# Kernel tuning notes

Hardware: AMD Instinct MI355X
Metric: run time of the kernel (lower is better)

Reference implementation:

```python
import jax, jax.numpy as jnp
import numpy as np

HEADS = 16
D_K = 64  # hidden_size // heads = 1024 // 16
SCALE = D_K ** 0.5


def setup_inputs() -> dict:
    key = jax.random.key(0)
    ks = jax.random.split(key, 7)
    B, S, D = 4, 2048, 1024
    H = 1024  # hidden_size
    O = 1024  # outputs_dims
    s = 0.02
    return {
        "query": jax.random.normal(ks[0], (B, S, D), dtype=jnp.float32),
        "key": jax.random.normal(ks[1], (B, S, D), dtype=jnp.float32),
        "value": jax.random.normal(ks[2], (B, S, D), dtype=jnp.float32),
        "Wq": jax.random.normal(ks[3], (D, H), dtype=jnp.float32) * s,
        "Wk": jax.random.normal(ks[4], (D, H), dtype=jnp.float32) * s,
        "Wv": jax.random.normal(ks[5], (D, H), dtype=jnp.float32) * s,
        "Wo": jax.random.normal(ks[6], (H, O), dtype=jnp.float32) * s,
    }


def reference(query, key, value, Wq, Wk, Wv, Wo):
    B, S, _ = query.shape
    # Dense projections with relu activation (as in the original module)
    q = jax.nn.relu(query @ Wq).reshape(B, S, HEADS, D_K)  # [B,S,H,dk]
    k = jax.nn.relu(key @ Wk).reshape(B, S, HEADS, D_K)
    v = jax.nn.relu(value @ Wv).reshape(B, S, HEADS, D_K)
    # scores: [B,H,Sq,Sk]
    scores = jnp.einsum('bqhd,bkhd->bhqk', q, k) / SCALE
    attn = jax.nn.softmax(scores, axis=-1)
    # attention-weighted values -> [B,Sq,H,dk] -> [B,Sq,H*dk]
    ctx = jnp.einsum('bhqk,bkhd->bqhd', attn, v).reshape(B, S, HEADS * D_K)
    out = jax.nn.relu(ctx @ Wo)
    return out
```

## Files before the change

kernel.cpp:

```cpp
#include <hip/hip_runtime.h>

typedef unsigned short u16;
typedef __bf16 bf16x8 __attribute__((ext_vector_type(8)));
typedef float f32x4 __attribute__((ext_vector_type(4)));
typedef u16 u16x8 __attribute__((ext_vector_type(8)));
typedef u16 u16x4 __attribute__((ext_vector_type(4)));

#define MFMA16(a, b, c) __builtin_amdgcn_mfma_f32_16x16x32_bf16(a, b, c, 0, 0, 0)

static constexpr float QSC = 0.18033688011112042f;

__device__ inline u16 f2bf(float f) {
  union { float f; unsigned u; } x; x.f = f;
  unsigned r = x.u + 0x7FFF + ((x.u >> 16) & 1);
  return (u16)(r >> 16);
}
__device__ inline u16 cvt_bf(float f) {
  __bf16 h = (__bf16)f; return __builtin_bit_cast(u16, h);
}
__device__ inline bf16x8 ld_frag(const u16* p) {
  return __builtin_bit_cast(bf16x8, *(const u16x8*)p);
}
__device__ inline void dma16(const u16* g, u16* l) {
  __builtin_amdgcn_global_load_lds(
      (const __attribute__((address_space(1))) unsigned*)g,
      (__attribute__((address_space(3))) unsigned*)l, 16, 0, 0);
}

#if __has_builtin(__builtin_amdgcn_exp2f)
#define EXP2(x) __builtin_amdgcn_exp2f(x)
#else
#define EXP2(x) exp2f(x)
#endif

__launch_bounds__(256)
__global__ void prep_w(const float* __restrict__ Wq, const float* __restrict__ Wk,
                       const float* __restrict__ Wv, const float* __restrict__ Wo,
                       u16* __restrict__ Wt) {
  __shared__ u16 T[64 * 72];
  const int z = blockIdx.z;
  const float* W = z == 0 ? Wq : z == 1 ? Wk : z == 2 ? Wv : Wo;
  u16* D = Wt + ((size_t)z << 20);
  const int k0 = blockIdx.y * 64, c0 = blockIdx.x * 64;
  const int tid = threadIdx.x;
  const int kr = tid >> 2, cs = (tid & 3) * 16;
  const float* src = W + (size_t)(k0 + kr) * 1024 + c0 + cs;
  float f[16];
#pragma unroll
  for (int i = 0; i < 4; ++i) *(float4*)&f[i * 4] = ((const float4*)src)[i];
#pragma unroll
  for (int i = 0; i < 16; ++i) T[(cs + i) * 72 + kr] = cvt_bf(f[i]);
  __syncthreads();
  const int nn = tid >> 2, ks = (tid & 3) * 16;
  u16* dst = D + (size_t)(c0 + nn) * 1024 + k0 + ks;
  *(u16x8*)dst = *(u16x8*)&T[nn * 72 + ks];
  *(u16x8*)(dst + 8) = *(u16x8*)&T[nn * 72 + ks + 8];
}

__launch_bounds__(256)
__global__ void prep_a(const float* __restrict__ q, const float* __restrict__ k,
                       const float* __restrict__ v, u16* __restrict__ dq,
                       u16* __restrict__ dk, u16* __restrict__ dv) {
  const int z = blockIdx.z;
  const float* s = z == 0 ? q : z == 1 ? k : v;
  u16* d = z == 0 ? dq : z == 1 ? dk : dv;
  for (size_t i = blockIdx.x * 256 + threadIdx.x; i < (size_t)1048576; i += 262144) {
    const float* g = s + i * 8;
    float4 f0 = *(const float4*)g, f1 = *(const float4*)(g + 4);
    u16x8 h;
    h[0] = cvt_bf(f0.x); h[1] = cvt_bf(f0.y); h[2] = cvt_bf(f0.z); h[3] = cvt_bf(f0.w);
    h[4] = cvt_bf(f1.x); h[5] = cvt_bf(f1.y); h[6] = cvt_bf(f1.z); h[7] = cvt_bf(f1.w);
    *(u16x8*)(d + i * 8) = h;
  }
}

__launch_bounds__(256)
__global__ void gemm_fwd(const u16* __restrict__ Aq, const u16* __restrict__ Ak,
                         const u16* __restrict__ Av, const u16* __restrict__ Wt,
                         u16* __restrict__ Qw, u16* __restrict__ Kw,
                         u16* __restrict__ Vw) {
  __shared__ u16 smem[8704];
  u16* Asm = smem;
  u16* Bsm = smem + 4096;
  const int z = blockIdx.z;
  const u16* A = z == 0 ? Aq : z == 1 ? Ak : Av;
  const u16* Bt = Wt + ((size_t)z << 20);
  u16* out = z == 0 ? Qw : z == 1 ? Kw : Vw;

  const int tid = threadIdx.x;
  const int lane = tid & 63, l15 = lane & 15, quad = lane >> 4;
  const int wv = tid >> 6, wm = wv & 1, wn = wv >> 1;
  const int m0 = (blockIdx.x * 8 + (blockIdx.y >> 3)) * 128;
  const int n0 = (blockIdx.y & 7) * 128;

  f32x4 acc[4][4] = {};

  for (int k0 = 0; k0 < 1024; k0 += 32) {
    __syncthreads();
#pragma unroll
    for (int t = 0; t < 2; ++t) {
      const int cb = t * 256 + wv * 64;
      const int c = cb + lane, mn = c & 127, kc = c >> 7;
      dma16(A + (size_t)(m0 + mn) * 1024 + k0 + kc * 8, &Asm[cb * 8]);
      dma16(Bt + (size_t)(n0 + mn) * 1024 + k0 + kc * 8, &Bsm[cb * 8]);
    }
    __syncthreads();
    bf16x8 a[4], b[4];
#pragma unroll
    for (int i = 0; i < 4; ++i)
      a[i] = ld_frag(&Asm[(quad * 128 + wm * 64 + i * 16 + l15) * 8]);
#pragma unroll
    for (int j = 0; j < 4; ++j)
      b[j] = ld_frag(&Bsm[(quad * 128 + wn * 64 + j * 16 + l15) * 8]);
#pragma unroll
    for (int i = 0; i < 4; ++i)
#pragma unroll
      for (int j = 0; j < 4; ++j)
        acc[i][j] = MFMA16(a[i], b[j], acc[i][j]);
  }

  if (z < 2) {
    const float sc = z == 0 ? QSC : 1.0f;
#pragma unroll
    for (int i = 0; i < 4; ++i)
#pragma unroll
      for (int j = 0; j < 4; ++j)
#pragma unroll
        for (int r = 0; r < 4; ++r) {
          float v = fmaxf(acc[i][j][r], 0.f) * sc;
          int m = m0 + wm * 64 + i * 16 + quad * 4 + r;
          int n = n0 + wn * 64 + j * 16 + l15;
          out[(size_t)m * 1024 + n] = f2bf(v);
        }
  } else {
    const int b = m0 >> 11, s0 = m0 & 2047;
#pragma unroll
    for (int half = 0; half < 2; ++half) {
      __syncthreads();
      if (wn == half) {
#pragma unroll
        for (int i = 0; i < 4; ++i)
#pragma unroll
          for (int j = 0; j < 4; ++j) {
            u16x4 pk;
#pragma unroll
            for (int r = 0; r < 4; ++r) pk[r] = f2bf(fmaxf(acc[i][j][r], 0.f));
            const int nn = j * 16 + l15;
            const int ml = wm * 64 + i * 16 + quad * 4;
            *(u16x4*)&smem[nn * 136 + ml] = pk;
          }
      }
      __syncthreads();
      const int h = (n0 + half * 64) >> 6;
      const int nn = tid >> 2, seg = (tid & 3) * 32;
      u16* dst = out + ((size_t)((b * 16 + h) * 64 + nn)) * 2048 + s0 + seg;
#pragma unroll
      for (int i2 = 0; i2 < 4; ++i2)
        *(u16x8*)&dst[i2 * 8] = *(u16x8*)&smem[nn * 136 + seg + i2 * 8];
    }
  }
}

__launch_bounds__(256)
__global__ void gemm_out(const u16* __restrict__ A, const u16* __restrict__ Bt,
                         float* __restrict__ out) {
  __shared__ u16 smem[8192];
  u16* Asm = smem;
  u16* Bsm = smem + 4096;
  const int tid = threadIdx.x;
  const int lane = tid & 63, l15 = lane & 15, quad = lane >> 4;
  const int wv = tid >> 6, wm = wv & 1, wn = wv >> 1;
  const int m0 = (blockIdx.x * 8 + (blockIdx.y >> 3)) * 128;
  const int n0 = (blockIdx.y & 7) * 128;
  f32x4 acc[4][4] = {};

  for (int k0 = 0; k0 < 1024; k0 += 32) {
    __syncthreads();
#pragma unroll
    for (int t = 0; t < 2; ++t) {
      const int cb = t * 256 + wv * 64;
      const int c = cb + lane, mn = c & 127, kc = c >> 7;
      dma16(A + (size_t)(m0 + mn) * 1024 + k0 + kc * 8, &Asm[cb * 8]);
      dma16(Bt + (size_t)(n0 + mn) * 1024 + k0 + kc * 8, &Bsm[cb * 8]);
    }
    __syncthreads();
    bf16x8 a[4], b[4];
#pragma unroll
    for (int i = 0; i < 4; ++i)
      a[i] = ld_frag(&Asm[(quad * 128 + wm * 64 + i * 16 + l15) * 8]);
#pragma unroll
    for (int j = 0; j < 4; ++j)
      b[j] = ld_frag(&Bsm[(quad * 128 + wn * 64 + j * 16 + l15) * 8]);
#pragma unroll
    for (int i = 0; i < 4; ++i)
#pragma unroll
      for (int j = 0; j < 4; ++j)
        acc[i][j] = MFMA16(a[i], b[j], acc[i][j]);
  }
#pragma unroll
  for (int i = 0; i < 4; ++i)
#pragma unroll
    for (int j = 0; j < 4; ++j)
#pragma unroll
      for (int r = 0; r < 4; ++r) {
        int m = m0 + wm * 64 + i * 16 + quad * 4 + r;
        int n = n0 + wn * 64 + j * 16 + l15;
        out[(size_t)m * 1024 + n] = fmaxf(acc[i][j][r], 0.f);
      }
}

__launch_bounds__(256, 3)
__global__ void attn(const u16* __restrict__ Q, const u16* __restrict__ K,
                     const u16* __restrict__ V, u16* __restrict__ ctx) {
  __shared__ u16 Ksm[2][4096];
  __shared__ u16 Vsm[2][4096];
  __shared__ u16 Psm[4][2048];

  const int tid = threadIdx.x;
  const int lane = tid & 63, l15 = lane & 15, quad = lane >> 4;
  const int wv = tid >> 6;
  const int bh = blockIdx.x, b = bh >> 4, h = bh & 15;
  const int q0 = blockIdx.y * 128 + wv * 32;

  const u16* Kb = K + ((size_t)b * 2048) * 1024 + h * 64;
  const u16* Vb = V + (size_t)bh * 64 * 2048;
  u16* Pw = Psm[wv];

  const int ck0 = tid, ck1 = 256 + tid;
  const u16* kg0 = Kb + (size_t)(ck0 & 63) * 1024 + (ck0 >> 6) * 8;
  const u16* kg1 = Kb + (size_t)(ck1 & 63) * 1024 + (ck1 >> 6) * 8;
  const u16* vg0 = Vb + (size_t)(ck0 & 63) * 2048 + (ck0 >> 6) * 8;
  const u16* vg1 = Vb + (size_t)(ck1 & 63) * 2048 + (ck1 >> 6) * 8;

  bf16x8 aq[2][2];
#pragma unroll
  for (int qh = 0; qh < 2; ++qh)
#pragma unroll
    for (int kk = 0; kk < 2; ++kk)
      aq[qh][kk] = ld_frag(Q + (size_t)(b * 2048 + q0 + qh * 16 + l15) * 1024 +
                           h * 64 + kk * 32 + quad * 8);

  f32x4 o[2][4] = {};
  float ls[2] = {0.f, 0.f};

  dma16(kg0, &Ksm[0][ck0 * 8]);
  dma16(kg1, &Ksm[0][ck1 * 8]);
  dma16(vg0, &Vsm[0][ck0 * 8]);
  dma16(vg1, &Vsm[0][ck1 * 8]);

#pragma unroll 1
  for (int t = 0; t < 32; ++t) {
    const int cur = t & 1, nxt = cur ^ 1;
    __syncthreads();

    if (t + 1 < 32) {
      const int kadv = (t + 1) * 64;
      dma16(kg0 + (size_t)kadv * 1024, &Ksm[nxt][ck0 * 8]);
      dma16(kg1 + (size_t)kadv * 1024, &Ksm[nxt][ck1 * 8]);
      dma16(vg0 + kadv, &Vsm[nxt][ck0 * 8]);
      dma16(vg1 + kadv, &Vsm[nxt][ck1 * 8]);
    }

    bf16x8 kf[2][4];
#pragma unroll
    for (int kk = 0; kk < 2; ++kk)
#pragma unroll
      for (int jj = 0; jj < 4; ++jj)
        kf[kk][jj] = ld_frag(&Ksm[cur][((kk * 4 + quad) * 64 + jj * 16 + l15) * 8]);

    f32x4 st[2][4] = {};
#pragma unroll
    for (int kk = 0; kk < 2; ++kk)
#pragma unroll
      for (int jj = 0; jj < 4; ++jj)
#pragma unroll
        for (int qh = 0; qh < 2; ++qh)
          st[qh][jj] = MFMA16(kf[kk][jj], aq[qh][kk], st[qh][jj]);

#pragma unroll
    for (int qh = 0; qh < 2; ++qh)
#pragma unroll
      for (int jj = 0; jj < 4; ++jj) {
        float p0 = EXP2(st[qh][jj][0]), p1 = EXP2(st[qh][jj][1]);
        float p2 = EXP2(st[qh][jj][2]), p3 = EXP2(st[qh][jj][3]);
        ls[qh] += (p0 + p1) + (p2 + p3);
        u16x4 pk;
        pk[0] = cvt_bf(p0); pk[1] = cvt_bf(p1);
        pk[2] = cvt_bf(p2); pk[3] = cvt_bf(p3);
        const int kc = jj * 2 + (quad >> 1);
        *(u16x4*)&Pw[(kc * 32 + qh * 16 + l15) * 8 + (quad & 1) * 4] = pk;
      }

#pragma unroll
    for (int kk = 0; kk < 2; ++kk) {
      bf16x8 pa[2];
#pragma unroll
      for (int qh = 0; qh < 2; ++qh)
        pa[qh] = ld_frag(&Pw[((kk * 4 + quad) * 32 + qh * 16 + l15) * 8]);
#pragma unroll
      for (int j = 0; j < 4; ++j) {
        bf16x8 vb = ld_frag(&Vsm[cur][((kk * 4 + quad) * 64 + j * 16 + l15) * 8]);
#pragma unroll
        for (int qh = 0; qh < 2; ++qh)
          o[qh][j] = MFMA16(vb, pa[qh], o[qh][j]);
      }
    }
  }

  float inv[2];
#pragma unroll
  for (int qh = 0; qh < 2; ++qh) {
    ls[qh] += __shfl_xor(ls[qh], 16, 64);
    ls[qh] += __shfl_xor(ls[qh], 32, 64);
    inv[qh] = 1.f / ls[qh];
  }

#pragma unroll
  for (int qh = 0; qh < 2; ++qh) {
    const int tok = b * 2048 + q0 + qh * 16 + l15;
#pragma unroll
    for (int j = 0; j < 4; ++j) {
      u16x4 pk;
#pragma unroll
      for (int r = 0; r < 4; ++r) pk[r] = cvt_bf(o[qh][j][r] * inv[qh]);
      *(u16x4*)&ctx[(size_t)tok * 1024 + h * 64 + j * 16 + quad * 4] = pk;
    }
  }
}

extern "C" void kernel_launch(void* const* d_in, const int* in_sizes, int n_in,
                              void* d_out, int out_size, void* d_ws, size_t ws_size,
                              hipStream_t stream) {
  const float* query = (const float*)d_in[0];
  const float* key   = (const float*)d_in[1];
  const float* value = (const float*)d_in[2];
  const float* Wq = (const float*)d_in[3];
  const float* Wk = (const float*)d_in[4];
  const float* Wv = (const float*)d_in[5];
  const float* Wo = (const float*)d_in[6];
  float* outp = (float*)d_out;

  u16* Wt  = (u16*)d_ws;
  u16* Awq = Wt + ((size_t)4 << 20);
  u16* Qw  = Awq + ((size_t)8 << 20);
  u16* Kw  = Qw + ((size_t)8 << 20);
  u16* Vt  = Kw + ((size_t)8 << 20);
  u16* Awk = (u16*)d_out;
  u16* Awv = Awk + ((size_t)8 << 20);
  u16* Cw  = Awq;

  prep_w<<<dim3(16, 16, 4), 256, 0, stream>>>(Wq, Wk, Wv, Wo, Wt);
  prep_a<<<dim3(1024, 1, 3), 256, 0, stream>>>(query, key, value, Awq, Awk, Awv);
  gemm_fwd<<<dim3(8, 64, 3), 256, 0, stream>>>(Awq, Awk, Awv, Wt, Qw, Kw, Vt);
  attn<<<dim3(64, 16), 256, 0, stream>>>(Qw, Kw, Vt, Cw);
  gemm_out<<<dim3(8, 64), 256, 0, stream>>>(Cw, Wt + ((size_t)3 << 20), outp);
}
```

Measured before the change: 400.8 us.

## Triple-buffer LDS in projection GEMMs with async prefetch two tiles ahead

Both projection GEMM kernels now keep three LDS buffers and issue global-to-LDS DMA loads two k-tiles ahead. Each iteration needs one barrier with explicit vmcnt/lgkmcnt waits instead of two __syncthreads per tile. This is meant to hide global load latency behind the MFMA work. LDS use per block triples, and launch bounds now request 3 blocks per CU, which may constrain registers and occupancy.

```diff
diff --git a/kernel.cpp b/kernel.cpp
--- a/kernel.cpp
+++ b/kernel.cpp
@@ -74,14 +74,12 @@
   }
 }
 
-__launch_bounds__(256)
+__launch_bounds__(256, 3)
 __global__ void gemm_fwd(const u16* __restrict__ Aq, const u16* __restrict__ Ak,
                          const u16* __restrict__ Av, const u16* __restrict__ Wt,
                          u16* __restrict__ Qw, u16* __restrict__ Kw,
                          u16* __restrict__ Vw) {
-  __shared__ u16 smem[8704];
-  u16* Asm = smem;
-  u16* Bsm = smem + 4096;
+  __shared__ u16 smem[24576];
   const int z = blockIdx.z;
   const u16* A = z == 0 ? Aq : z == 1 ? Ak : Av;
   const u16* Bt = Wt + ((size_t)z << 20);
@@ -93,31 +91,57 @@
   const int m0 = (blockIdx.x * 8 + (blockIdx.y >> 3)) * 128;
   const int n0 = (blockIdx.y & 7) * 128;
 
+  const int c0 = tid, c1 = 256 + tid;
+  const u16* ga0 = A + (size_t)(m0 + (c0 & 127)) * 1024 + (c0 >> 7) * 8;
+  const u16* ga1 = A + (size_t)(m0 + (c1 & 127)) * 1024 + (c1 >> 7) * 8;
+  const u16* gb0 = Bt + (size_t)(n0 + (c0 & 127)) * 1024 + (c0 >> 7) * 8;
+  const u16* gb1 = Bt + (size_t)(n0 + (c1 & 127)) * 1024 + (c1 >> 7) * 8;
+  const int la0 = (wv * 64) * 8, la1 = (256 + wv * 64) * 8;
+
   f32x4 acc[4][4] = {};
 
-  for (int k0 = 0; k0 < 1024; k0 += 32) {
-    __syncthreads();
-#pragma unroll
-    for (int t = 0; t < 2; ++t) {
-      const int cb = t * 256 + wv * 64;
-      const int c = cb + lane, mn = c & 127, kc = c >> 7;
-      dma16(A + (size_t)(m0 + mn) * 1024 + k0 + kc * 8, &Asm[cb * 8]);
-      dma16(Bt + (size_t)(n0 + mn) * 1024 + k0 + kc * 8, &Bsm[cb * 8]);
-    }
-    __syncthreads();
+#define STAGE(kt, bo)                                   \
+  do {                                                  \
+    const int k0_ = (kt) * 32;                          \
+    dma16(ga0 + k0_, &smem[(bo) + la0]);                \
+    dma16(gb0 + k0_, &smem[(bo) + 4096 + la0]);         \
+    dma16(ga1 + k0_, &smem[(bo) + la1]);                \
+    dma16(gb1 + k0_, &smem[(bo) + 4096 + la1]);         \
+  } while (0)
+
+  STAGE(0, 0);
+  STAGE(1, 8192);
+  asm volatile("s_waitcnt vmcnt(4)" ::: "memory");
+  __builtin_amdgcn_sched_barrier(0);
+  __builtin_amdgcn_s_barrier();
+
+  int bo0 = 0, bo1 = 8192, bo2 = 16384;
+  const int offA = (quad * 128 + wm * 64 + l15) * 8;
+  const int offB = (quad * 128 + wn * 64 + l15) * 8;
+#pragma unroll 1
+  for (int t = 0; t < 32; ++t) {
+    if (t < 30) STAGE(t + 2, bo2);
+    const u16* Ab = smem + bo0;
+    const u16* Bb = smem + bo0 + 4096;
     bf16x8 a[4], b[4];
 #pragma unroll
-    for (int i = 0; i < 4; ++i)
-      a[i] = ld_frag(&Asm[(quad * 128 + wm * 64 + i * 16 + l15) * 8]);
-#pragma unroll
-    for (int j = 0; j < 4; ++j)
-      b[j] = ld_frag(&Bsm[(quad * 128 + wn * 64 + j * 16 + l15) * 8]);
+    for (int i = 0; i < 4; ++i) a[i] = ld_frag(Ab + offA + i * 128);
+#pragma unroll
+    for (int j = 0; j < 4; ++j) b[j] = ld_frag(Bb + offB + j * 128);
+    if (t < 30)
+      asm volatile("s_waitcnt vmcnt(4) lgkmcnt(0)" ::: "memory");
+    else
+      asm volatile("s_waitcnt vmcnt(0) lgkmcnt(0)" ::: "memory");
+    __builtin_amdgcn_sched_barrier(0);
+    __builtin_amdgcn_s_barrier();
 #pragma unroll
     for (int i = 0; i < 4; ++i)
 #pragma unroll
       for (int j = 0; j < 4; ++j)
         acc[i][j] = MFMA16(a[i], b[j], acc[i][j]);
-  }
+    const int tb = bo0; bo0 = bo1; bo1 = bo2; bo2 = tb;
+  }
+#undef STAGE
 
   if (z < 2) {
     const float sc = z == 0 ? QSC : 1.0f;
@@ -161,42 +185,68 @@
   }
 }
 
-__launch_bounds__(256)
+__launch_bounds__(256, 3)
 __global__ void gemm_out(const u16* __restrict__ A, const u16* __restrict__ Bt,
                          float* __restrict__ out) {
-  __shared__ u16 smem[8192];
-  u16* Asm = smem;
-  u16* Bsm = smem + 4096;
+  __shared__ u16 smem[24576];
   const int tid = threadIdx.x;
   const int lane = tid & 63, l15 = lane & 15, quad = lane >> 4;
   const int wv = tid >> 6, wm = wv & 1, wn = wv >> 1;
   const int m0 = (blockIdx.x * 8 + (blockIdx.y >> 3)) * 128;
   const int n0 = (blockIdx.y & 7) * 128;
+
+  const int c0 = tid, c1 = 256 + tid;
+  const u16* ga0 = A + (size_t)(m0 + (c0 & 127)) * 1024 + (c0 >> 7) * 8;
+  const u16* ga1 = A + (size_t)(m0 + (c1 & 127)) * 1024 + (c1 >> 7) * 8;
+  const u16* gb0 = Bt + (size_t)(n0 + (c0 & 127)) * 1024 + (c0 >> 7) * 8;
+  const u16* gb1 = Bt + (size_t)(n0 + (c1 & 127)) * 1024 + (c1 >> 7) * 8;
+  const int la0 = (wv * 64) * 8, la1 = (256 + wv * 64) * 8;
+
   f32x4 acc[4][4] = {};
 
-  for (int k0 = 0; k0 < 1024; k0 += 32) {
-    __syncthreads();
-#pragma unroll
-    for (int t = 0; t < 2; ++t) {
-      const int cb = t * 256 + wv * 64;
-      const int c = cb + lane, mn = c & 127, kc = c >> 7;
-      dma16(A + (size_t)(m0 + mn) * 1024 + k0 + kc * 8, &Asm[cb * 8]);
-      dma16(Bt + (size_t)(n0 + mn) * 1024 + k0 + kc * 8, &Bsm[cb * 8]);
-    }
-    __syncthreads();
+#define STAGE(kt, bo)                                   \
+  do {                                                  \
+    const int k0_ = (kt) * 32;                          \
+    dma16(ga0 + k0_, &smem[(bo) + la0]);                \
+    dma16(gb0 + k0_, &smem[(bo) + 4096 + la0]);         \
+    dma16(ga1 + k0_, &smem[(bo) + la1]);                \
+    dma16(gb1 + k0_, &smem[(bo) + 4096 + la1]);         \
+  } while (0)
+
+  STAGE(0, 0);
+  STAGE(1, 8192);
+  asm volatile("s_waitcnt vmcnt(4)" ::: "memory");
+  __builtin_amdgcn_sched_barrier(0);
+  __builtin_amdgcn_s_barrier();
+
+  int bo0 = 0, bo1 = 8192, bo2 = 16384;
+  const int offA = (quad * 128 + wm * 64 + l15) * 8;
+  const int offB = (quad * 128 + wn * 64 + l15) * 8;
+#pragma unroll 1
+  for (int t = 0; t < 32; ++t) {
+    if (t < 30) STAGE(t + 2, bo2);
+    const u16* Ab = smem + bo0;
+    const u16* Bb = smem + bo0 + 4096;
     bf16x8 a[4], b[4];
 #pragma unroll
-    for (int i = 0; i < 4; ++i)
-      a[i] = ld_frag(&Asm[(quad * 128 + wm * 64 + i * 16 + l15) * 8]);
-#pragma unroll
-    for (int j = 0; j < 4; ++j)
-      b[j] = ld_frag(&Bsm[(quad * 128 + wn * 64 + j * 16 + l15) * 8]);
+    for (int i = 0; i < 4; ++i) a[i] = ld_frag(Ab + offA + i * 128);
+#pragma unroll
+    for (int j = 0; j < 4; ++j) b[j] = ld_frag(Bb + offB + j * 128);
+    if (t < 30)
+      asm volatile("s_waitcnt vmcnt(4) lgkmcnt(0)" ::: "memory");
+    else
+      asm volatile("s_waitcnt vmcnt(0) lgkmcnt(0)" ::: "memory");
+    __builtin_amdgcn_sched_barrier(0);
+    __builtin_amdgcn_s_barrier();
 #pragma unroll
     for (int i = 0; i < 4; ++i)
 #pragma unroll
       for (int j = 0; j < 4; ++j)
         acc[i][j] = MFMA16(a[i], b[j], acc[i][j]);
-  }
+    const int tb = bo0; bo0 = bo1; bo1 = bo2; bo2 = tb;
+  }
+#undef STAGE
+
 #pragma unroll
   for (int i = 0; i < 4; ++i)
 #pragma unroll
```

Result: no change. 401.5 us (+0.2%).
